# Performance work log

Measured on AMD Instinct MI355X. Metric: run time of the kernel, lower is better.

## Reference

```python
import jax, jax.numpy as jnp
import numpy as np


def setup_inputs() -> dict:
    key = jax.random.key(0)
    k1, k2 = jax.random.split(key)
    B, H, W, C = 32, 32, 32, 256
    N_EMBED = 1024
    z = jax.random.normal(k1, (B, H, W, C), dtype=jnp.float32)
    emb_weights = jax.random.normal(k2, (N_EMBED, C), dtype=jnp.float32)
    return {"z": z, "emb_weights": emb_weights}


def reference(z, emb_weights):
    # z: (B,H,W,C) -> flatten to (N, C)
    B = z.shape[0]
    C = z.shape[-1]
    z_flat = z.reshape(-1, C)  # (N, C)
    # Squared euclidean distance via ||z||^2 + ||e||^2 - 2 z.e^T
    distance = (
        jnp.sum(z_flat ** 2, axis=1, keepdims=True)          # (N, 1)
        + jnp.sum(emb_weights ** 2, axis=1)                   # (n_embed,)
        - 2.0 * jnp.dot(z_flat, emb_weights.T)                # (N, n_embed)
    )
    min_encoding_indices = jnp.argmin(distance, axis=1)       # (N,)
    z_q = emb_weights[min_encoding_indices].reshape(z.shape)  # (B,H,W,C)
    min_encoding_indices = min_encoding_indices.reshape(B, -1)
    return z_q, min_encoding_indices
```

## Files before the change

kernel.cpp:

```cpp
#include <hip/hip_runtime.h>

#define C_DIM 256
#define NCODE 1024
#define MARGIN 0.02f

typedef __bf16 bf16x8 __attribute__((ext_vector_type(8)));
typedef float f32x4 __attribute__((ext_vector_type(4)));

#define WS_ENORM 0
#define WS_META  4096
#define WS_RLIST 8192
#define WS_BP    139264

#define GLOAD_LDS16(g, s)                                                            \
  __builtin_amdgcn_global_load_lds(                                                  \
      (const __attribute__((address_space(1))) unsigned int*)(g),                    \
      (__attribute__((address_space(3))) unsigned int*)(s), 16, 0, 0)

__device__ __forceinline__ void bf16split(float x, unsigned short& h, unsigned short& l) {
    unsigned u  = __float_as_uint(x);
    unsigned rh = (u + 0x7FFFu + ((u >> 16) & 1u)) & 0xFFFF0000u;
    float    lf = x - __uint_as_float(rh);
    unsigned ul = __float_as_uint(lf);
    h = (unsigned short)(rh >> 16);
    l = (unsigned short)((ul + 0x7FFFu + ((ul >> 16) & 1u)) >> 16);
}

__global__ __launch_bounds__(256) void prep_misc_kernel(const float* __restrict__ emb,
                                                        float* __restrict__ enorm,
                                                        unsigned* __restrict__ meta) {
    int gid = blockIdx.x * 256 + threadIdx.x;
    if (gid == 0) meta[0] = 0u;
    int row = gid >> 6, lane = gid & 63;
    float4 v = reinterpret_cast<const float4*>(emb)[(size_t)row * 64 + lane];
    float s = v.x * v.x + v.y * v.y + v.z * v.z + v.w * v.w;
    #pragma unroll
    for (int off = 32; off; off >>= 1) s += __shfl_xor(s, off, 64);
    if (lane == 0) enorm[row] = s;
}

__global__ __launch_bounds__(256) void prep_b_kernel(const float* __restrict__ emb,
                                                     unsigned short* __restrict__ bp) {
    int tid = blockIdx.x * 256 + threadIdx.x;
    int j   = tid >> 5;
    int u   = tid & 31;
    int kc  = u >> 2, lg = u & 3;
    const float* src = emb + (size_t)j * C_DIM + kc * 32 + lg * 8;
    float4 v0 = *reinterpret_cast<const float4*>(src);
    float4 v1 = *reinterpret_cast<const float4*>(src + 4);
    float vs[8] = {v0.x, v0.y, v0.z, v0.w, v1.x, v1.y, v1.z, v1.w};
    unsigned short h[8], l[8];
    #pragma unroll
    for (int k = 0; k < 8; ++k) bf16split(vs[k], h[k], l[k]);
    int chunk = j >> 5, nf = (j >> 4) & 1, lr = j & 15;
    int lane  = lg * 16 + lr;
    size_t base = (size_t)chunk * 16384 + (size_t)(nf * 8 + kc) * 512 + lane * 8;
    uint4 hp, lp;
    hp.x = (unsigned)h[0] | ((unsigned)h[1] << 16);
    hp.y = (unsigned)h[2] | ((unsigned)h[3] << 16);
    hp.z = (unsigned)h[4] | ((unsigned)h[5] << 16);
    hp.w = (unsigned)h[6] | ((unsigned)h[7] << 16);
    lp.x = (unsigned)l[0] | ((unsigned)l[1] << 16);
    lp.y = (unsigned)l[2] | ((unsigned)l[3] << 16);
    lp.z = (unsigned)l[4] | ((unsigned)l[5] << 16);
    lp.w = (unsigned)l[6] | ((unsigned)l[7] << 16);
    *reinterpret_cast<uint4*>(bp + base)             = hp;
    *reinterpret_cast<uint4*>(bp + base + 16 * 512)  = lp;
}

__global__ __launch_bounds__(512, 2) void vq_main_kernel(
    const float* __restrict__ z, const unsigned short* __restrict__ bp,
    const float* __restrict__ emb, const float* __restrict__ enorm,
    float* __restrict__ zq, float* __restrict__ idx_out,
    unsigned* __restrict__ meta, unsigned* __restrict__ rlist) {
    __shared__ alignas(16) unsigned short Bds[2][16384];
    __shared__ float en_s[NCODE];
    __shared__ float mv1[128][2], mv2[128][2];
    __shared__ unsigned mi[128][2];
    __shared__ unsigned codes_l[128];

    const int t    = threadIdx.x;
    const int w    = t >> 6;
    const int lane = t & 63;
    const int lr   = lane & 15, lg = lane >> 4;
    const int wm   = w >> 1;
    const int ng   = w & 1;
    const long r0  = (long)blockIdx.x * 128;

    {
        const unsigned short* src = bp;
        #pragma unroll
        for (int round = 0; round < 4; ++round) {
            int f = round * 8 + w;
            GLOAD_LDS16(src + (size_t)f * 512 + lane * 8, &Bds[0][f * 512]);
        }
    }
    en_s[t]       = enorm[t];
    en_s[t + 512] = enorm[t + 512];

    bf16x8 ah[2][8], al[2][8];
    #pragma unroll
    for (int m = 0; m < 2; ++m) {
        const float* zr = z + (r0 + wm * 32 + m * 16 + lr) * C_DIM + lg * 8;
        #pragma unroll
        for (int kc = 0; kc < 8; ++kc) {
            float4 v0 = *reinterpret_cast<const float4*>(zr + kc * 32);
            float4 v1 = *reinterpret_cast<const float4*>(zr + kc * 32 + 4);
            float vs[8] = {v0.x, v0.y, v0.z, v0.w, v1.x, v1.y, v1.z, v1.w};
            unsigned short hv[8], lv[8];
            #pragma unroll
            for (int jj = 0; jj < 8; ++jj) bf16split(vs[jj], hv[jj], lv[jj]);
            unsigned hp[4] = {
                (unsigned)hv[0] | ((unsigned)hv[1] << 16), (unsigned)hv[2] | ((unsigned)hv[3] << 16),
                (unsigned)hv[4] | ((unsigned)hv[5] << 16), (unsigned)hv[6] | ((unsigned)hv[7] << 16)};
            unsigned lp[4] = {
                (unsigned)lv[0] | ((unsigned)lv[1] << 16), (unsigned)lv[2] | ((unsigned)lv[3] << 16),
                (unsigned)lv[4] | ((unsigned)lv[5] << 16), (unsigned)lv[6] | ((unsigned)lv[7] << 16)};
            ah[m][kc] = __builtin_bit_cast(bf16x8, *reinterpret_cast<uint4*>(hp));
            al[m][kc] = __builtin_bit_cast(bf16x8, *reinterpret_cast<uint4*>(lp));
        }
    }

    float b1[2][4], b2[2][4]; unsigned i1[2][4];
    #pragma unroll
    for (int m = 0; m < 2; ++m)
        #pragma unroll
        for (int r = 0; r < 4; ++r) { b1[m][r] = 3.4e38f; b2[m][r] = 3.4e38f; i1[m][r] = 0; }

    for (int c = 0; c < 32; ++c) {
        const int cur = c & 1;
        __syncthreads();
        if (c < 31) {
            const unsigned short* src = bp + (size_t)(c + 1) * 16384;
            #pragma unroll
            for (int round = 0; round < 4; ++round) {
                int f = round * 8 + w;
                GLOAD_LDS16(src + (size_t)f * 512 + lane * 8, &Bds[cur ^ 1][f * 512]);
            }
            asm volatile("s_waitcnt vmcnt(4)" ::: "memory");
        } else {
            asm volatile("s_waitcnt vmcnt(0)" ::: "memory");
        }
        __syncthreads();

        f32x4 hh0 = {0.f,0.f,0.f,0.f}, hh1 = {0.f,0.f,0.f,0.f};
        f32x4 hl0 = {0.f,0.f,0.f,0.f}, hl1 = {0.f,0.f,0.f,0.f};
        f32x4 lh0 = {0.f,0.f,0.f,0.f}, lh1 = {0.f,0.f,0.f,0.f};
        const unsigned short* bb = &Bds[cur][(ng * 8) * 512 + lane * 8];
        #pragma unroll
        for (int kc = 0; kc < 8; ++kc) {
            bf16x8 bh = *reinterpret_cast<const bf16x8*>(bb + kc * 512);
            bf16x8 bl = *reinterpret_cast<const bf16x8*>(bb + (16 + kc) * 512);
            hh0 = __builtin_amdgcn_mfma_f32_16x16x32_bf16(ah[0][kc], bh, hh0, 0, 0, 0);
            hh1 = __builtin_amdgcn_mfma_f32_16x16x32_bf16(ah[1][kc], bh, hh1, 0, 0, 0);
            lh0 = __builtin_amdgcn_mfma_f32_16x16x32_bf16(al[0][kc], bh, lh0, 0, 0, 0);
            lh1 = __builtin_amdgcn_mfma_f32_16x16x32_bf16(al[1][kc], bh, lh1, 0, 0, 0);
            hl0 = __builtin_amdgcn_mfma_f32_16x16x32_bf16(ah[0][kc], bl, hl0, 0, 0, 0);
            hl1 = __builtin_amdgcn_mfma_f32_16x16x32_bf16(ah[1][kc], bl, hl1, 0, 0, 0);
        }

        const float    en   = en_s[c * 32 + ng * 16 + lr];
        const unsigned code = (unsigned)(c * 32 + ng * 16 + lr);
        #pragma unroll
        for (int r = 0; r < 4; ++r) {
            float d0 = fmaf(-2.f, hh0[r] + hl0[r] + lh0[r], en);
            if (d0 < b1[0][r]) { b2[0][r] = b1[0][r]; b1[0][r] = d0; i1[0][r] = code; }
            else if (d0 < b2[0][r]) { b2[0][r] = d0; }
            float d1 = fmaf(-2.f, hh1[r] + hl1[r] + lh1[r], en);
            if (d1 < b1[1][r]) { b2[1][r] = b1[1][r]; b1[1][r] = d1; i1[1][r] = code; }
            else if (d1 < b2[1][r]) { b2[1][r] = d1; }
        }
    }

    #pragma unroll
    for (int m = 0; m < 2; ++m)
        #pragma unroll
        for (int r = 0; r < 4; ++r) {
            float v1 = b1[m][r], v2 = b2[m][r]; unsigned j1 = i1[m][r];
            #pragma unroll
            for (int off = 8; off; off >>= 1) {
                float    ov1 = __shfl_xor(v1, off, 64);
                float    ov2 = __shfl_xor(v2, off, 64);
                unsigned oj1 = (unsigned)__shfl_xor((int)j1, off, 64);
                if (ov1 < v1 || (ov1 == v1 && oj1 < j1)) {
                    v2 = fminf(v1, ov2); v1 = ov1; j1 = oj1;
                } else {
                    v2 = fminf(v2, ov1);
                }
            }
            if (lr == 0) {
                int rowl = wm * 32 + m * 16 + lg * 4 + r;
                mv1[rowl][ng] = v1; mv2[rowl][ng] = v2; mi[rowl][ng] = j1;
            }
        }
    __syncthreads();
    if (t < 128) {
        float B1 = mv1[t][0], B2 = mv2[t][0]; unsigned I1 = mi[t][0];
        float o1 = mv1[t][1], o2 = mv2[t][1]; unsigned O1 = mi[t][1];
        if (o1 < B1 || (o1 == B1 && O1 < I1)) { B2 = fminf(B1, o2); B1 = o1; I1 = O1; }
        else                                  { B2 = fminf(B2, o1); }
        long row = r0 + t;
        idx_out[row] = (float)I1;
        codes_l[t]   = I1;
        if (B2 - B1 <= MARGIN) rlist[atomicAdd(meta, 1u)] = (unsigned)row;
    }
    __syncthreads();

    {
        int rowl = t >> 2, q = t & 3;
        unsigned code = codes_l[rowl];
        const float4* ep = reinterpret_cast<const float4*>(emb) + (size_t)code * 64 + q * 16;
        float4*       op = reinterpret_cast<float4*>(zq) + ((size_t)(r0 + rowl)) * 64 + q * 16;
        #pragma unroll
        for (int jj = 0; jj < 16; ++jj) op[jj] = ep[jj];
    }
}

__global__ __launch_bounds__(256) void rescue_kernel(
    const float* __restrict__ z, const float* __restrict__ emb,
    const float* __restrict__ enorm, const unsigned* __restrict__ meta,
    const unsigned* __restrict__ rlist, float* __restrict__ zq,
    float* __restrict__ idx_out) {
    __shared__ float zrow[C_DIM];
    __shared__ float rd[256];
    __shared__ unsigned rix[256];
    const unsigned cnt = meta[0];
    for (unsigned li = blockIdx.x; li < cnt; li += gridDim.x) {
        unsigned row = rlist[li];
        __syncthreads();
        if (threadIdx.x < 64) {
            float4 v = reinterpret_cast<const float4*>(z)[(size_t)row * 64 + threadIdx.x];
            reinterpret_cast<float4*>(zrow)[threadIdx.x] = v;
        }
        __syncthreads();
        const int c = threadIdx.x;
        float a0 = 0.f, a1 = 0.f, a2 = 0.f, a3 = 0.f;
        const float4* zp = reinterpret_cast<const float4*>(zrow);
        const float4* e0 = reinterpret_cast<const float4*>(emb + (size_t)(c)       * C_DIM);
        const float4* e1 = reinterpret_cast<const float4*>(emb + (size_t)(c + 256) * C_DIM);
        const float4* e2 = reinterpret_cast<const float4*>(emb + (size_t)(c + 512) * C_DIM);
        const float4* e3 = reinterpret_cast<const float4*>(emb + (size_t)(c + 768) * C_DIM);
        #pragma unroll 8
        for (int k = 0; k < 64; ++k) {
            float4 z4 = zp[k];
            float4 f0 = e0[k], f1 = e1[k], f2 = e2[k], f3 = e3[k];
            a0 = fmaf(z4.x, f0.x, a0); a0 = fmaf(z4.y, f0.y, a0);
            a0 = fmaf(z4.z, f0.z, a0); a0 = fmaf(z4.w, f0.w, a0);
            a1 = fmaf(z4.x, f1.x, a1); a1 = fmaf(z4.y, f1.y, a1);
            a1 = fmaf(z4.z, f1.z, a1); a1 = fmaf(z4.w, f1.w, a1);
            a2 = fmaf(z4.x, f2.x, a2); a2 = fmaf(z4.y, f2.y, a2);
            a2 = fmaf(z4.z, f2.z, a2); a2 = fmaf(z4.w, f2.w, a2);
            a3 = fmaf(z4.x, f3.x, a3); a3 = fmaf(z4.y, f3.y, a3);
            a3 = fmaf(z4.z, f3.z, a3); a3 = fmaf(z4.w, f3.w, a3);
        }
        float d0 = fmaf(-2.f, a0, enorm[c]);
        float d1 = fmaf(-2.f, a1, enorm[c + 256]);
        float d2 = fmaf(-2.f, a2, enorm[c + 512]);
        float d3 = fmaf(-2.f, a3, enorm[c + 768]);
        float bd = d0; unsigned bi = (unsigned)c;
        if (d1 < bd) { bd = d1; bi = (unsigned)(c + 256); }
        if (d2 < bd) { bd = d2; bi = (unsigned)(c + 512); }
        if (d3 < bd) { bd = d3; bi = (unsigned)(c + 768); }
        rd[threadIdx.x] = bd; rix[threadIdx.x] = bi;
        __syncthreads();
        for (int s = 128; s; s >>= 1) {
            if (threadIdx.x < (unsigned)s) {
                float od = rd[threadIdx.x + s]; unsigned oi = rix[threadIdx.x + s];
                if (od < rd[threadIdx.x] ||
                    (od == rd[threadIdx.x] && oi < rix[threadIdx.x])) {
                    rd[threadIdx.x] = od; rix[threadIdx.x] = oi;
                }
            }
            __syncthreads();
        }
        unsigned code = rix[0];
        if (threadIdx.x < 64) {
            float4 v = reinterpret_cast<const float4*>(emb)[(size_t)code * 64 + threadIdx.x];
            reinterpret_cast<float4*>(zq)[(size_t)row * 64 + threadIdx.x] = v;
        }
        if (threadIdx.x == 0) idx_out[row] = (float)code;
    }
}

extern "C" void kernel_launch(void* const* d_in, const int* in_sizes, int n_in,
                              void* d_out, int out_size, void* d_ws, size_t ws_size,
                              hipStream_t stream) {
    const float* z   = (const float*)d_in[0];
    const float* emb = (const float*)d_in[1];
    const int n = in_sizes[0] / C_DIM;

    float* zq      = (float*)d_out;
    float* idx_out = zq + (size_t)n * C_DIM;

    char* ws = (char*)d_ws;
    float*          enorm = (float*)(ws + WS_ENORM);
    unsigned*       meta  = (unsigned*)(ws + WS_META);
    unsigned*       rlist = (unsigned*)(ws + WS_RLIST);
    unsigned short* bp    = (unsigned short*)(ws + WS_BP);

    prep_misc_kernel<<<256, 256, 0, stream>>>(emb, enorm, meta);
    prep_b_kernel<<<128, 256, 0, stream>>>(emb, bp);
    vq_main_kernel<<<n / 128, 512, 0, stream>>>(z, bp, emb, enorm, zq, idx_out,
                                                meta, rlist);
    rescue_kernel<<<256, 256, 0, stream>>>(z, emb, enorm, meta, rlist, zq, idx_out);
}
```

Baseline: 135.9 us.

## Split codebook search across two blocks per row tile and add finalize-gather kernel

The main VQ kernel now splits the 1024-code search into two halves handled by separate blocks, doubling the grid so more blocks are available to fill the GPU. Each block writes per-row partial best and second-best distances and indices to workspace. A new finalize kernel merges the two halves, writes indices, queues near-tie rows for rescue and gathers the embedding rows into the output. The cost is that each row's z data is loaded and split twice, plus an extra launch and a partial-result round trip through memory. Ties between halves go to the first half, since codes there have lower indices.

```diff
diff --git a/kernel.cpp b/kernel.cpp
--- a/kernel.cpp
+++ b/kernel.cpp
@@ -11,6 +11,8 @@
 #define WS_META  4096
 #define WS_RLIST 8192
 #define WS_BP    139264
+#define WS_PB    1187840
+#define WS_PBI   1712128
 
 #define GLOAD_LDS16(g, s)                                                            \
   __builtin_amdgcn_global_load_lds(                                                  \
@@ -70,14 +72,12 @@
 
 __global__ __launch_bounds__(512, 2) void vq_main_kernel(
     const float* __restrict__ z, const unsigned short* __restrict__ bp,
-    const float* __restrict__ emb, const float* __restrict__ enorm,
-    float* __restrict__ zq, float* __restrict__ idx_out,
-    unsigned* __restrict__ meta, unsigned* __restrict__ rlist) {
+    const float* __restrict__ enorm, float2* __restrict__ pb,
+    unsigned* __restrict__ pbi) {
     __shared__ alignas(16) unsigned short Bds[2][16384];
-    __shared__ float en_s[NCODE];
+    __shared__ float en_s[512];
     __shared__ float mv1[128][2], mv2[128][2];
     __shared__ unsigned mi[128][2];
-    __shared__ unsigned codes_l[128];
 
     const int t    = threadIdx.x;
     const int w    = t >> 6;
@@ -85,18 +85,16 @@
     const int lr   = lane & 15, lg = lane >> 4;
     const int wm   = w >> 1;
     const int ng   = w & 1;
-    const long r0  = (long)blockIdx.x * 128;
-
-    {
-        const unsigned short* src = bp;
-        #pragma unroll
-        for (int round = 0; round < 4; ++round) {
-            int f = round * 8 + w;
-            GLOAD_LDS16(src + (size_t)f * 512 + lane * 8, &Bds[0][f * 512]);
-        }
-    }
-    en_s[t]       = enorm[t];
-    en_s[t + 512] = enorm[t + 512];
+    const int  nh  = blockIdx.x & 1;
+    const long r0  = (long)(blockIdx.x >> 1) * 128;
+    const unsigned short* bph = bp + (size_t)nh * 16 * 16384;
+
+    #pragma unroll
+    for (int round = 0; round < 4; ++round) {
+        int f = round * 8 + w;
+        GLOAD_LDS16(bph + (size_t)f * 512 + lane * 8, &Bds[0][f * 512]);
+    }
+    if (t < 512) en_s[t] = enorm[nh * 512 + t];
 
     bf16x8 ah[2][8], al[2][8];
     #pragma unroll
@@ -127,11 +125,11 @@
         #pragma unroll
         for (int r = 0; r < 4; ++r) { b1[m][r] = 3.4e38f; b2[m][r] = 3.4e38f; i1[m][r] = 0; }
 
-    for (int c = 0; c < 32; ++c) {
+    for (int c = 0; c < 16; ++c) {
         const int cur = c & 1;
         __syncthreads();
-        if (c < 31) {
-            const unsigned short* src = bp + (size_t)(c + 1) * 16384;
+        if (c < 15) {
+            const unsigned short* src = bph + (size_t)(c + 1) * 16384;
             #pragma unroll
             for (int round = 0; round < 4; ++round) {
                 int f = round * 8 + w;
@@ -160,7 +158,7 @@
         }
 
         const float    en   = en_s[c * 32 + ng * 16 + lr];
-        const unsigned code = (unsigned)(c * 32 + ng * 16 + lr);
+        const unsigned code = (unsigned)(nh * 512 + c * 32 + ng * 16 + lr);
         #pragma unroll
         for (int r = 0; r < 4; ++r) {
             float d0 = fmaf(-2.f, hh0[r] + hl0[r] + lh0[r], en);
@@ -199,21 +197,29 @@
         float o1 = mv1[t][1], o2 = mv2[t][1]; unsigned O1 = mi[t][1];
         if (o1 < B1 || (o1 == B1 && O1 < I1)) { B2 = fminf(B1, o2); B1 = o1; I1 = O1; }
         else                                  { B2 = fminf(B2, o1); }
-        long row = r0 + t;
+        pb [(r0 + t) * 2 + nh] = make_float2(B1, B2);
+        pbi[(r0 + t) * 2 + nh] = I1;
+    }
+}
+
+__global__ __launch_bounds__(256) void finalize_gather_kernel(
+    const float* __restrict__ emb, const float2* __restrict__ pb,
+    const unsigned* __restrict__ pbi, float* __restrict__ zq,
+    float* __restrict__ idx_out, unsigned* __restrict__ meta,
+    unsigned* __restrict__ rlist) {
+    const long row = (long)blockIdx.x * 4 + (threadIdx.x >> 6);
+    const int lane = threadIdx.x & 63;
+    float2   p0 = pb [row * 2 + 0], p1 = pb [row * 2 + 1];
+    unsigned j0 = pbi[row * 2 + 0], j1 = pbi[row * 2 + 1];
+    float B1, B2; unsigned I1;
+    if (p1.x < p0.x) { B1 = p1.x; I1 = j1; B2 = fminf(p0.x, p1.y); }
+    else             { B1 = p0.x; I1 = j0; B2 = fminf(p0.y, p1.x); }
+    if (lane == 0) {
         idx_out[row] = (float)I1;
-        codes_l[t]   = I1;
         if (B2 - B1 <= MARGIN) rlist[atomicAdd(meta, 1u)] = (unsigned)row;
     }
-    __syncthreads();
-
-    {
-        int rowl = t >> 2, q = t & 3;
-        unsigned code = codes_l[rowl];
-        const float4* ep = reinterpret_cast<const float4*>(emb) + (size_t)code * 64 + q * 16;
-        float4*       op = reinterpret_cast<float4*>(zq) + ((size_t)(r0 + rowl)) * 64 + q * 16;
-        #pragma unroll
-        for (int jj = 0; jj < 16; ++jj) op[jj] = ep[jj];
-    }
+    float4 v = reinterpret_cast<const float4*>(emb)[(size_t)I1 * 64 + lane];
+    reinterpret_cast<float4*>(zq)[row * 64 + lane] = v;
 }
 
 __global__ __launch_bounds__(256) void rescue_kernel(
@@ -297,10 +303,13 @@
     unsigned*       meta  = (unsigned*)(ws + WS_META);
     unsigned*       rlist = (unsigned*)(ws + WS_RLIST);
     unsigned short* bp    = (unsigned short*)(ws + WS_BP);
+    float2*         pb    = (float2*)(ws + WS_PB);
+    unsigned*       pbi   = (unsigned*)(ws + WS_PBI);
 
     prep_misc_kernel<<<256, 256, 0, stream>>>(emb, enorm, meta);
     prep_b_kernel<<<128, 256, 0, stream>>>(emb, bp);
-    vq_main_kernel<<<n / 128, 512, 0, stream>>>(z, bp, emb, enorm, zq, idx_out,
-                                                meta, rlist);
+    vq_main_kernel<<<(n / 128) * 2, 512, 0, stream>>>(z, bp, enorm, pb, pbi);
+    finalize_gather_kernel<<<n / 4, 256, 0, stream>>>(emb, pb, pbi, zq, idx_out,
+                                                      meta, rlist);
     rescue_kernel<<<256, 256, 0, stream>>>(z, emb, enorm, meta, rlist, zq, idx_out);
 }
```

Measured after the change: 149.3 us. 9.8% more time.
